# Performance work log

Hardware: AMD Instinct MI355X
Metric: run time of the kernel (lower is better)

Reference implementation:

```python
import jax, jax.numpy as jnp
import numpy as np

HIDDEN = 768
HEADS = 12
ORDERS = 3
NEG = -1e9


def setup_inputs() -> dict:
    key = jax.random.key(0)
    ks = jax.random.split(key, 16)
    B, N = 8, 512
    s = 0.02
    inp = {
        "v": jax.random.normal(ks[0], (B, N, HIDDEN), jnp.float32),
        "k": jax.random.normal(ks[1], (B, N, HIDDEN), jnp.float32),
        "q": jax.random.normal(ks[2], (B, N, HIDDEN), jnp.float32),
        "masks": jax.random.bernoulli(ks[3], 0.1, (ORDERS, B, 1, N, N)),
        "tau": 1,
        "training": 0,
        "Wv": jax.random.normal(ks[4], (HIDDEN, HIDDEN), jnp.float32) * s,
        "bv": jnp.zeros((HIDDEN,), jnp.float32),
        "Wk": jax.random.normal(ks[5], (HIDDEN, HIDDEN), jnp.float32) * s,
        "bk": jnp.zeros((HIDDEN,), jnp.float32),
        "Wq": jax.random.normal(ks[6], (HIDDEN, HIDDEN), jnp.float32) * s,
        "bq": jnp.zeros((HIDDEN,), jnp.float32),
        "Wm": jax.random.normal(ks[7], (HIDDEN, HIDDEN), jnp.float32) * s,
        "bm": jnp.zeros((HIDDEN,), jnp.float32),
        "pool_w": jax.random.normal(ks[8], (HIDDEN, 1), jnp.float32) * s,
        "pool_b": jnp.zeros((1,), jnp.float32),
        "mlp_w1": jax.random.normal(ks[9], (HIDDEN, HIDDEN // 2), jnp.float32) * s,
        "mlp_w2": jax.random.normal(ks[10], (HIDDEN // 2, ORDERS), jnp.float32) * s,
        "mlp_b2": jnp.zeros((ORDERS,), jnp.float32),
    }
    return inp


def _soft_routing(x, pool_w, pool_b, mlp_w1, mlp_w2, mlp_b2):
    # pooling='fc': masked attention pooling over sequence, then 2-layer MLP + softmax
    pad = (jnp.sum(jnp.abs(x), axis=-1) == 0)[:, :, None]        # [B, N, 1]
    scores = x @ pool_w + pool_b                                  # [B, N, 1]
    scores = jnp.where(pad, NEG, scores)
    scores = jax.nn.softmax(scores, axis=1)
    pooled = jnp.sum(x * scores, axis=1)                          # [B, HIDDEN]
    logits = jax.nn.relu(pooled @ mlp_w1) @ mlp_w2 + mlp_b2       # [B, L]
    return jax.nn.softmax(logits, axis=-1)


def reference(v, k, q, masks, tau, training, Wv, bv, Wk, bk, Wq, bq, Wm, bm,
              pool_w, pool_b, mlp_w1, mlp_w2, mlp_b2):
    B, N, _ = q.shape
    dk = HIDDEN // HEADS
    alphas = _soft_routing(v, pool_w, pool_b, mlp_w1, mlp_w2, mlp_b2)  # [B, L]

    def split_heads(x):
        return x.reshape(B, N, HEADS, dk).transpose(0, 2, 1, 3)  # [B, H, N, dk]

    vh = split_heads(v @ Wv + bv)
    kh = split_heads(k @ Wk + bk)
    qh = split_heads(q @ Wq + bq)

    scores = jnp.einsum('bhnd,bhmd->bhnm', qh, kh) / jnp.sqrt(jnp.float32(dk))
    # masks: [L, B, 1, N, N] broadcast over heads -> att_list [L, B, H, N, N]
    masked = jnp.where(masks[:, :, :, :, :], NEG, scores[None])
    att_list = jax.nn.softmax(masked, axis=-1)                    # [L, B, H, N, N]
    att_map = jnp.einsum('bl,lbhnm->bhnm', alphas, att_list)
    atted = jnp.einsum('bhnm,bhmd->bhnd', att_map, vh)
    atted = atted.transpose(0, 2, 1, 3).reshape(B, N, HIDDEN)
    return atted @ Wm + bm
```

## Files before the change

kernel.cpp:

```cpp
#include <hip/hip_runtime.h>
#include <hip/hip_bf16.h>
#include <stdint.h>


typedef __bf16 bf16x8 __attribute__((ext_vector_type(8)));
typedef float f32x4 __attribute__((ext_vector_type(4)));

#define NEGV -1e9f

__device__ __forceinline__ float b2f(unsigned short h) {
    union { unsigned int u; float f; } x; x.u = ((unsigned int)h) << 16; return x.f;
}
__device__ __forceinline__ unsigned short f2b(float f) {
    union { float f; unsigned int u; } x; x.f = f;
    unsigned int u = x.u + 0x7FFFu + ((x.u >> 16) & 1u);
    return (unsigned short)(u >> 16);
}
__device__ __forceinline__ unsigned int packbf(unsigned int u0, unsigned int u1) {
    unsigned int r0 = (u0 + 0x7FFFu + ((u0 >> 16) & 1u)) >> 16;
    unsigned int r1 = (u1 + 0x7FFFu + ((u1 >> 16) & 1u)) & 0xFFFF0000u;
    return r0 | r1;
}
__device__ __forceinline__ uint4 load8bf(const void* base, size_t elemOff, int isF32) {
    if (!isF32) return *(const uint4*)((const unsigned short*)base + elemOff);
    const uint4* f = (const uint4*)((const float*)base + elemOff);
    uint4 a = f[0], b = f[1];
    uint4 r;
    r.x = packbf(a.x, a.y);
    r.y = packbf(a.z, a.w);
    r.z = packbf(b.x, b.y);
    r.w = packbf(b.z, b.w);
    return r;
}
__device__ __forceinline__ float loadF(const void* p, int idx, int isF32) {
    return isF32 ? ((const float*)p)[idx] : b2f(((const unsigned short*)p)[idx]);
}

__global__ void sniff_kernel(const unsigned int* __restrict__ mp,
                             const unsigned int* __restrict__ vp,
                             const unsigned int* __restrict__ wp,
                             int* __restrict__ flags)
{
    __shared__ int oki, oku, okf, badv, badw;
    if (threadIdx.x == 0) { oki = 1; oku = 1; okf = 1; badv = 0; badw = 0; }
    __syncthreads();
    int li = 1, lu = 1, lf = 1, bv = 0, bw = 0;
    for (int i = threadIdx.x; i < 16384; i += 256) {
        unsigned int w = mp[i];
        if (w > 1u) li = 0;
        if (w & 0xFEFEFEFEu) lu = 0;
        if (w != 0u && w != 0x3F800000u) lf = 0;
    }
    for (int i = threadIdx.x; i < 8192; i += 256) {
        unsigned int w = vp[i];
        float f0 = b2f((unsigned short)(w & 0xFFFF));
        float f1 = b2f((unsigned short)(w >> 16));
        if (!(fabsf(f0) < 1e4f) || !(fabsf(f1) < 1e4f)) bv = 1;
        w = wp[i];
        f0 = b2f((unsigned short)(w & 0xFFFF));
        f1 = b2f((unsigned short)(w >> 16));
        if (!(fabsf(f0) < 1e4f) || !(fabsf(f1) < 1e4f)) bw = 1;
    }
    if (!li) atomicAnd(&oki, 0);
    if (!lu) atomicAnd(&oku, 0);
    if (!lf) atomicAnd(&okf, 0);
    if (bv) atomicOr(&badv, 1);
    if (bw) atomicOr(&badw, 1);
    __syncthreads();
    if (threadIdx.x == 0) {
        flags[0] = oki ? 0 : (oku ? 1 : (okf ? 2 : 3));
        flags[1] = badv;
        flags[2] = badw;
    }
}

__global__ __launch_bounds__(256) void conv_act_kernel(
        const void* __restrict__ v, const void* __restrict__ k,
        const void* __restrict__ q, const int* __restrict__ flags,
        unsigned short* __restrict__ vb, unsigned short* __restrict__ kb,
        unsigned short* __restrict__ qb)
{
    const int dtV = flags[1];
    const int which = blockIdx.y;
    const void* src = (which == 0) ? v : (which == 1) ? k : q;
    unsigned short* dst = (which == 0) ? vb : (which == 1) ? kb : qb;
    size_t off = ((size_t)blockIdx.x * 256 + threadIdx.x) * 8;
    uint4 r = load8bf(src, off, dtV);
    *(uint4*)(dst + off) = r;
}

__global__ __launch_bounds__(256) void conv_wt_kernel(
        const void* __restrict__ W0, const void* __restrict__ W1,
        const void* __restrict__ W2, const void* __restrict__ W3,
        const int* __restrict__ flags,
        unsigned short* __restrict__ T0, unsigned short* __restrict__ T1,
        unsigned short* __restrict__ T2, unsigned short* __restrict__ T3)
{
    __shared__ unsigned short tile[64][65];
    const int t = threadIdx.x;
    const int dtW = flags[2];
    const int which = blockIdx.y;
    const void* W = (which == 0) ? W0 : (which == 1) ? W1 : (which == 2) ? W2 : W3;
    unsigned short* T = (which == 0) ? T0 : (which == 1) ? T1 : (which == 2) ? T2 : T3;
    const int tk = (blockIdx.x / 12) << 6;
    const int tn = (blockIdx.x % 12) << 6;
    #pragma unroll
    for (int i = 0; i < 16; i++) {
        int idx = (i << 8) + t;
        int r = idx >> 6, c = idx & 63;
        tile[r][c] = f2b(loadF(W, (tk + r) * 768 + tn + c, dtW));
    }
    __syncthreads();
    #pragma unroll
    for (int i = 0; i < 16; i++) {
        int idx = (i << 8) + t;
        int rn = idx >> 6, ck = idx & 63;
        T[(size_t)(tn + rn) * 768 + tk + ck] = tile[ck][rn];
    }
}

__global__ __launch_bounds__(256) void pack_kernel(
        const void* __restrict__ masks, const int* __restrict__ flags,
        unsigned int* __restrict__ pm)
{
    __shared__ unsigned char flg[32 * 512];
    const int t = threadIdx.x;
    const int mode = flags[0];
    const size_t e0 = (size_t)blockIdx.x * (32 * 512);
    if (mode == 0 || mode == 2) {
        const uint4* p = (const uint4*)((const unsigned int*)masks + e0);
        for (int i = t; i < 4096; i += 256) {
            uint4 u = p[i];
            int base = i << 2;
            flg[base + 0] = u.x ? 1 : 0;
            flg[base + 1] = u.y ? 1 : 0;
            flg[base + 2] = u.z ? 1 : 0;
            flg[base + 3] = u.w ? 1 : 0;
        }
    } else if (mode == 1) {
        const uint4* p = (const uint4*)((const unsigned char*)masks + e0);
        for (int i = t; i < 1024; i += 256) {
            uint4 u = p[i];
            unsigned int uu[4] = {u.x, u.y, u.z, u.w};
            int base = i << 4;
            #pragma unroll
            for (int k2 = 0; k2 < 4; k2++)
                #pragma unroll
                for (int bb = 0; bb < 4; bb++)
                    flg[base + k2 * 4 + bb] = ((uu[k2] >> (bb * 8)) & 0xFFu) ? 1 : 0;
        }
    } else {
        const uint4* p = (const uint4*)((const unsigned short*)masks + e0);
        for (int i = t; i < 2048; i += 256) {
            uint4 u = p[i];
            unsigned int uu[4] = {u.x, u.y, u.z, u.w};
            int base = i << 3;
            #pragma unroll
            for (int k2 = 0; k2 < 4; k2++) {
                flg[base + k2 * 2 + 0] = (uu[k2] & 0xFFFFu) ? 1 : 0;
                flg[base + k2 * 2 + 1] = (uu[k2] >> 16) ? 1 : 0;
            }
        }
    }
    __syncthreads();
    for (int widx = t; widx < 512; widx += 256) {
        int rl = widx >> 4, lm = widx & 15;
        unsigned int bits = 0;
        #pragma unroll
        for (int g = 0; g < 32; g++)
            bits |= ((unsigned int)(flg[rl * 512 + (g << 4) + lm] & 1)) << g;
        pm[(size_t)blockIdx.x * 512 + widx] = bits;
    }
}

__global__ __launch_bounds__(256) void route_score_kernel(
        const void* __restrict__ v, const void* __restrict__ pool_w,
        const void* __restrict__ pool_b, const int* __restrict__ flags,
        float* __restrict__ scores)
{
    __shared__ float pw[768];
    const int t = threadIdx.x;
    const int b = blockIdx.x >> 3, ch = blockIdx.x & 7;
    const int dtV = flags[1], dtW = flags[2];
    for (int d = t; d < 768; d += 256) pw[d] = loadF(pool_w, d, dtW);
    __syncthreads();
    const int r = t >> 2, c4 = t & 3;
    const int n = (ch << 6) + r;
    float dot = 0.f, asum = 0.f;
    if (!dtV) {
        const unsigned int* vr = (const unsigned int*)v + ((size_t)(b * 512 + n)) * 384;
        for (int j = 0; j < 96; j++) {
            int p = c4 + (j << 2);
            unsigned int u = vr[p];
            float f0 = b2f((unsigned short)(u & 0xFFFF));
            float f1 = b2f((unsigned short)(u >> 16));
            asum += fabsf(f0) + fabsf(f1);
            dot += f0 * pw[2 * p] + f1 * pw[2 * p + 1];
        }
    } else {
        const float* vf = (const float*)v + ((size_t)(b * 512 + n)) * 768;
        for (int j = 0; j < 48; j++) {
            float4 u = ((const float4*)vf)[c4 + (j << 2)];
            int e = (c4 + (j << 2)) << 2;
            asum += fabsf(u.x) + fabsf(u.y) + fabsf(u.z) + fabsf(u.w);
            dot += u.x * pw[e] + u.y * pw[e + 1] + u.z * pw[e + 2] + u.w * pw[e + 3];
        }
    }
    dot += __shfl_xor(dot, 1); dot += __shfl_xor(dot, 2);
    asum += __shfl_xor(asum, 1); asum += __shfl_xor(asum, 2);
    if (c4 == 0)
        scores[b * 512 + n] = (asum == 0.f) ? NEGV : dot + loadF(pool_b, 0, dtW);
}

__global__ __launch_bounds__(512) void route_softmax_kernel(
        const float* __restrict__ scores, float* __restrict__ scs)
{
    __shared__ float red[8];
    const int t = threadIdx.x, b = blockIdx.x;
    float scv = scores[b * 512 + t];
    float mx = scv;
    #pragma unroll
    for (int off = 1; off < 64; off <<= 1) mx = fmaxf(mx, __shfl_xor(mx, off));
    if ((t & 63) == 0) red[t >> 6] = mx;
    __syncthreads();
    float M = red[0];
    #pragma unroll
    for (int i = 1; i < 8; i++) M = fmaxf(M, red[i]);
    float e = __expf(scv - M);
    __syncthreads();
    float sm = e;
    #pragma unroll
    for (int off = 1; off < 64; off <<= 1) sm += __shfl_xor(sm, off);
    if ((t & 63) == 0) red[t >> 6] = sm;
    __syncthreads();
    float SS = 0.f;
    #pragma unroll
    for (int i = 0; i < 8; i++) SS += red[i];
    scs[b * 512 + t] = e / SS;
}

__global__ __launch_bounds__(256) void route_pool_kernel(
        const void* __restrict__ v, const int* __restrict__ flags,
        const float* __restrict__ scs, float* __restrict__ ppart)
{
    __shared__ float ps[64];
    const int t = threadIdx.x;
    const int ch = blockIdx.x, b = blockIdx.y;
    const int dtV = flags[1];
    if (t < 64) ps[t] = scs[b * 512 + (ch << 6) + t];
    __syncthreads();
    const int d0 = t * 3;
    float a0 = 0.f, a1 = 0.f, a2 = 0.f;
    if (!dtV) {
        const unsigned short* vb = (const unsigned short*)v
            + ((size_t)(b * 512 + (ch << 6))) * 768 + d0;
        #pragma unroll 4
        for (int r = 0; r < 64; r++) {
            float p = ps[r];
            a0 += b2f(vb[0]) * p; a1 += b2f(vb[1]) * p; a2 += b2f(vb[2]) * p;
            vb += 768;
        }
    } else {
        const float* vb = (const float*)v + ((size_t)(b * 512 + (ch << 6))) * 768 + d0;
        #pragma unroll 4
        for (int r = 0; r < 64; r++) {
            float p = ps[r];
            a0 += vb[0] * p; a1 += vb[1] * p; a2 += vb[2] * p;
            vb += 768;
        }
    }
    float* o = ppart + ((size_t)(b * 8 + ch)) * 768 + d0;
    o[0] = a0; o[1] = a1; o[2] = a2;
}

__global__ __launch_bounds__(256) void route_hid_kernel(
        const void* __restrict__ w1, const void* __restrict__ w2,
        const int* __restrict__ flags, const float* __restrict__ ppart,
        float* __restrict__ plog)
{
    __shared__ float pool[768];
    __shared__ float red[4][32];
    const int t = threadIdx.x;
    const int jc = blockIdx.x, b = blockIdx.y;
    const int dtW = flags[2];
    for (int d = t; d < 768; d += 256) {
        float a = 0.f;
        #pragma unroll
        for (int c = 0; c < 8; c++) a += ppart[((size_t)(b * 8 + c)) * 768 + d];
        pool[d] = a;
    }
    __syncthreads();
    const int jo = (t & 3) << 3;
    const int dr = t >> 2;
    float acc[8];
    #pragma unroll
    for (int j = 0; j < 8; j++) acc[j] = 0.f;
    for (int it = 0; it < 12; it++) {
        int d = (it << 6) + dr;
        float pv = pool[d];
        size_t off = (size_t)d * 384 + (jc << 5) + jo;
        if (!dtW) {
            uint4 u = *(const uint4*)((const unsigned short*)w1 + off);
            unsigned int uu[4] = {u.x, u.y, u.z, u.w};
            #pragma unroll
            for (int j2 = 0; j2 < 4; j2++) {
                acc[2 * j2]     += pv * b2f((unsigned short)(uu[j2] & 0xFFFF));
                acc[2 * j2 + 1] += pv * b2f((unsigned short)(uu[j2] >> 16));
            }
        } else {
            const float4* f = (const float4*)((const float*)w1 + off);
            float4 u0 = f[0], u1 = f[1];
            acc[0] += pv * u0.x; acc[1] += pv * u0.y;
            acc[2] += pv * u0.z; acc[3] += pv * u0.w;
            acc[4] += pv * u1.x; acc[5] += pv * u1.y;
            acc[6] += pv * u1.z; acc[7] += pv * u1.w;
        }
    }
    #pragma unroll
    for (int off = 4; off < 64; off <<= 1)
        #pragma unroll
        for (int j = 0; j < 8; j++) acc[j] += __shfl_xor(acc[j], off);
    const int w = t >> 6, lane = t & 63;
    if (lane < 4) {
        #pragma unroll
        for (int j = 0; j < 8; j++) red[w][lane * 8 + j] = acc[j];
    }
    __syncthreads();
    if (t < 32) {
        float h = red[0][t] + red[1][t] + red[2][t] + red[3][t];
        h = fmaxf(h, 0.f);
        int jg = (jc << 5) + t;
        float l0 = h * loadF(w2, jg * 3 + 0, dtW);
        float l1 = h * loadF(w2, jg * 3 + 1, dtW);
        float l2 = h * loadF(w2, jg * 3 + 2, dtW);
        #pragma unroll
        for (int off = 1; off < 32; off <<= 1) {
            l0 += __shfl_xor(l0, off);
            l1 += __shfl_xor(l1, off);
            l2 += __shfl_xor(l2, off);
        }
        if (t == 0) {
            float* o = plog + ((size_t)(b * 12 + jc)) * 3;
            o[0] = l0; o[1] = l1; o[2] = l2;
        }
    }
}

__global__ __launch_bounds__(64) void route_alpha_kernel(
        const void* __restrict__ b2, const int* __restrict__ flags,
        const float* __restrict__ plog, float* __restrict__ alphas)
{
    const int t = threadIdx.x, b = blockIdx.x;
    if (t == 0) {
        const int dtW = flags[2];
        float lg[3];
        #pragma unroll
        for (int l = 0; l < 3; l++) {
            float a = loadF(b2, l, dtW);
            for (int jc = 0; jc < 12; jc++) a += plog[((size_t)(b * 12 + jc)) * 3 + l];
            lg[l] = a;
        }
        float mm = fmaxf(lg[0], fmaxf(lg[1], lg[2]));
        float e0 = __expf(lg[0] - mm), e1 = __expf(lg[1] - mm), e2 = __expf(lg[2] - mm);
        float ss = e0 + e1 + e2;
        alphas[b * 3 + 0] = e0 / ss;
        alphas[b * 3 + 1] = e1 / ss;
        alphas[b * 3 + 2] = e2 / ss;
    }
}

__global__ __launch_bounds__(256) void gemm3_kernel(
        const unsigned short* __restrict__ X0, const unsigned short* __restrict__ X1,
        const unsigned short* __restrict__ X2,
        const unsigned short* __restrict__ W0, const unsigned short* __restrict__ W1,
        const unsigned short* __restrict__ W2,
        const void* __restrict__ bias0, const void* __restrict__ bias1,
        const void* __restrict__ bias2,
        const int* __restrict__ flags,
        void* __restrict__ dst0, void* __restrict__ dst1, void* __restrict__ dst2,
        int m0, int m1, int m2)
{
    __shared__ unsigned short smem[8192];
    unsigned short* At = smem;
    unsigned short* Bt = smem + 4096;
    const int t = threadIdx.x;
    const int which = blockIdx.y;
    const unsigned short* X  = (which == 0) ? X0 : (which == 1) ? X1 : X2;
    const unsigned short* WT = (which == 0) ? W0 : (which == 1) ? W1 : W2;
    const void* bias = (which == 0) ? bias0 : (which == 1) ? bias1 : bias2;
    void* dst = (which == 0) ? dst0 : (which == 1) ? dst1 : dst2;
    const int mode = (which == 0) ? m0 : (which == 1) ? m1 : m2;

    const int id = blockIdx.x;
    const int bx = id >> 6, by = id & 63;
    const int row0 = by << 6, col0 = bx << 6;
    const int w = t >> 6, lane = t & 63, quad = lane >> 4, lm = lane & 15;
    const int r0 = t >> 3, c0 = (t & 7) << 3;
    const int wr0 = r0 * 64 + (c0 ^ ((r0 & 7) << 3));
    const int dtW = flags[2];
    const int dtOut = flags[1];

    const unsigned short* xp  = X  + (size_t)(row0 + r0) * 768 + c0;
    const unsigned short* xp2 = xp + 32 * 768;
    const unsigned short* wp  = WT + (size_t)(col0 + r0) * 768 + c0;
    const unsigned short* wp2 = wp + 32 * 768;

    uint4 a0 = *(const uint4*)xp,  a1 = *(const uint4*)xp2;
    uint4 g0 = *(const uint4*)wp,  g1 = *(const uint4*)wp2;

    f32x4 acc[4];
    #pragma unroll
    for (int i = 0; i < 4; i++) acc[i] = (f32x4){0.f, 0.f, 0.f, 0.f};

    const int am = (w << 4) + lm;
    const int abase = am * 64, akey = (am & 7) << 3;

    for (int k0 = 0;;) {
        __syncthreads();
        *(uint4*)&At[wr0] = a0;        *(uint4*)&At[wr0 + 2048] = a1;
        *(uint4*)&Bt[wr0] = g0;        *(uint4*)&Bt[wr0 + 2048] = g1;
        __syncthreads();
        k0 += 64;
        if (k0 < 768) {
            a0 = *(const uint4*)(xp + k0);  a1 = *(const uint4*)(xp2 + k0);
            g0 = *(const uint4*)(wp + k0);  g1 = *(const uint4*)(wp2 + k0);
        }
        #pragma unroll
        for (int ks = 0; ks < 2; ks++) {
            int ko = (quad << 3) + (ks << 5);
            bf16x8 afr = *(const bf16x8*)&At[abase + (ko ^ akey)];
            #pragma unroll
            for (int t4 = 0; t4 < 4; t4++) {
                int bn = (t4 << 4) + lm;
                bf16x8 bfr = *(const bf16x8*)&Bt[bn * 64 + (ko ^ ((bn & 7) << 3))];
                acc[t4] = __builtin_amdgcn_mfma_f32_16x16x32_bf16(afr, bfr, acc[t4], 0, 0, 0);
            }
        }
        if (k0 >= 768) break;
    }

    if (mode == 1 && dtOut) {
        #pragma unroll
        for (int t4 = 0; t4 < 4; t4++) {
            int col = col0 + (t4 << 4) + lm;
            float bsv = loadF(bias, col, dtW);
            #pragma unroll
            for (int rg = 0; rg < 4; rg++) {
                int row = row0 + (w << 4) + (quad << 2) + rg;
                ((float*)dst)[(size_t)row * 768 + col] = acc[t4][rg] + bsv;
            }
        }
        return;
    }

    __syncthreads();
    #pragma unroll
    for (int t4 = 0; t4 < 4; t4++) {
        int colL = (t4 << 4) + lm;
        float bsv = loadF(bias, col0 + colL, dtW);
        #pragma unroll
        for (int rg = 0; rg < 4; rg++) {
            int rowL = (w << 4) + (quad << 2) + rg;
            unsigned short hv = f2b(acc[t4][rg] + bsv);
            if (mode == 2) smem[colL * 72 + rowL] = hv;
            else           smem[rowL * 72 + colL] = hv;
        }
    }
    __syncthreads();
    const int g = t >> 2, cc = (t & 3) << 4;
    uint4 o0 = *(const uint4*)&smem[g * 72 + cc];
    uint4 o1 = *(const uint4*)&smem[g * 72 + cc + 8];
    unsigned short* o;
    if (mode == 0) {
        int b = row0 >> 9, n0b = row0 & 511, h = col0 >> 6;
        o = (unsigned short*)dst + ((size_t)(b * 12 + h) * 512 + n0b + g) * 64 + cc;
    } else if (mode == 2) {
        int b = row0 >> 9, n0b = row0 & 511, h = col0 >> 6;
        o = (unsigned short*)dst + ((size_t)(b * 12 + h) * 64 + g) * 512 + n0b + cc;
    } else {
        o = (unsigned short*)dst + (size_t)(row0 + g) * 768 + col0 + cc;
    }
    *(uint4*)o = o0;
    *(uint4*)(o + 8) = o1;
}

__global__ __launch_bounds__(256) void attn_kernel(
        const unsigned short* __restrict__ qh, const unsigned short* __restrict__ kh,
        const unsigned short* __restrict__ vT, const unsigned int* __restrict__ pm,
        const float* __restrict__ alphas, unsigned short* __restrict__ atted)
{
    __shared__ unsigned short P[16 * 512];
    __shared__ float Zp[4][16][3];
    __shared__ unsigned short Ost[16 * 72];
    const int t = threadIdx.x;
    const int w = t >> 6, lane = t & 63, quad = lane >> 4, lm = lane & 15;
    const int id = blockIdx.x;
    const int bh = id % 96, qb = id / 96;
    const int b = bh / 12, h = bh % 12;
    const int n0 = qb << 4;

    const unsigned short* qrow = qh + ((size_t)(bh * 512 + n0 + lm)) * 64 + (quad << 3);
    bf16x8 qa0 = *(const bf16x8*)qrow;
    bf16x8 qa1 = *(const bf16x8*)(qrow + 32);
    f32x4 acc[8];
    #pragma unroll
    for (int i = 0; i < 8; i++) acc[i] = (f32x4){0.f, 0.f, 0.f, 0.f};
    const unsigned short* kb0 = kh + ((size_t)(bh * 512 + (w << 7) + lm)) * 64 + (quad << 3);
    #pragma unroll
    for (int nt = 0; nt < 8; nt++) {
        const unsigned short* kr = kb0 + nt * (16 * 64);
        bf16x8 k0 = *(const bf16x8*)kr;
        bf16x8 k1 = *(const bf16x8*)(kr + 32);
        acc[nt] = __builtin_amdgcn_mfma_f32_16x16x32_bf16(qa0, k0, acc[nt], 0, 0, 0);
        acc[nt] = __builtin_amdgcn_mfma_f32_16x16x32_bf16(qa1, k1, acc[nt], 0, 0, 0);
    }

    float al[3];
    #pragma unroll
    for (int l = 0; l < 3; l++) al[l] = alphas[b * 3 + l];

    #pragma unroll
    for (int nt = 0; nt < 8; nt++)
        #pragma unroll
        for (int rg = 0; rg < 4; rg++)
            acc[nt][rg] = __expf(acc[nt][rg] * 0.125f);

    unsigned int mkw[4][3];
    #pragma unroll
    for (int rg = 0; rg < 4; rg++)
        #pragma unroll
        for (int l = 0; l < 3; l++)
            mkw[rg][l] = pm[((size_t)((l << 3) + b) * 512 + n0 + (quad << 2) + rg) * 16 + lm]
                         >> (w << 3);

    #pragma unroll
    for (int rg = 0; rg < 4; rg++) {
        float z0 = 0.f, z1 = 0.f, z2 = 0.f;
        #pragma unroll
        for (int nt = 0; nt < 8; nt++) {
            float e = acc[nt][rg];
            if (!((mkw[rg][0] >> nt) & 1)) z0 += e;
            if (!((mkw[rg][1] >> nt) & 1)) z1 += e;
            if (!((mkw[rg][2] >> nt) & 1)) z2 += e;
        }
        #pragma unroll
        for (int off = 1; off < 16; off <<= 1) {
            z0 += __shfl_xor(z0, off);
            z1 += __shfl_xor(z1, off);
            z2 += __shfl_xor(z2, off);
        }
        if (lm == 0) {
            int row = (quad << 2) + rg;
            Zp[w][row][0] = z0; Zp[w][row][1] = z1; Zp[w][row][2] = z2;
        }
    }
    __syncthreads();

    #pragma unroll
    for (int rg = 0; rg < 4; rg++) {
        int row = (quad << 2) + rg;
        float coef[3]; float addu = 0.f;
        #pragma unroll
        for (int l = 0; l < 3; l++) {
            float Z = Zp[0][row][l] + Zp[1][row][l] + Zp[2][row][l] + Zp[3][row][l];
            if (Z > 0.f) coef[l] = al[l] / Z;
            else { coef[l] = 0.f; addu += al[l] * (1.0f / 512.0f); }
        }
        #pragma unroll
        for (int nt = 0; nt < 8; nt++) {
            int g = (w << 3) + nt;
            float p = addu;
            float e = acc[nt][rg];
            if (!((mkw[rg][0] >> nt) & 1)) p += coef[0] * e;
            if (!((mkw[rg][1] >> nt) & 1)) p += coef[1] * e;
            if (!((mkw[rg][2] >> nt) & 1)) p += coef[2] * e;
            int c = (g << 4) + lm;
            int chunk = c >> 3, j = c & 7;
            P[row * 512 + (((chunk ^ (row & 7))) << 3) + j] = f2b(p);
        }
    }
    __syncthreads();

    f32x4 accO = (f32x4){0.f, 0.f, 0.f, 0.f};
    const unsigned short* vb = vT + ((size_t)(bh * 64 + (w << 4) + lm)) * 512 + (quad << 3);
    #pragma unroll
    for (int ks = 0; ks < 16; ks++) {
        bf16x8 pa = *(const bf16x8*)&P[lm * 512 + ((((ks << 2) + quad) ^ (lm & 7)) << 3)];
        bf16x8 vf = *(const bf16x8*)(vb + (ks << 5));
        accO = __builtin_amdgcn_mfma_f32_16x16x32_bf16(pa, vf, accO, 0, 0, 0);
    }
    #pragma unroll
    for (int rg = 0; rg < 4; rg++)
        Ost[((quad << 2) + rg) * 72 + (w << 4) + lm] = f2b(accO[rg]);
    __syncthreads();
    const int r2 = t >> 4, c4 = t & 15;
    uint2 val = *(const uint2*)&Ost[r2 * 72 + (c4 << 2)];
    *(uint2*)&atted[((size_t)(b * 512 + n0 + r2)) * 768 + (h << 6) + (c4 << 2)] = val;
}

extern "C" void kernel_launch(void* const* d_in, const int* in_sizes, int n_in,
                              void* d_out, int out_size, void* d_ws, size_t ws_size,
                              hipStream_t stream)
{
    const void* v  = d_in[0];
    const void* k  = d_in[1];
    const void* q  = d_in[2];
    const void* mk = d_in[3];
    const void* Wv = d_in[6];
    const void* bv = d_in[7];
    const void* Wk = d_in[8];
    const void* bk = d_in[9];
    const void* Wq = d_in[10];
    const void* bq = d_in[11];
    const void* Wm = d_in[12];
    const void* bm = d_in[13];
    const void* pool_w = d_in[14];
    const void* pool_b = d_in[15];
    const void* w1 = d_in[16];
    const void* w2 = d_in[17];
    const void* b2 = d_in[18];

    char* ws = (char*)d_ws;
    int*   flags  = (int*)ws;
    float* alphas = (float*)(ws + 256);
    float* scores = (float*)(ws + 512);
    float* scs    = (float*)(ws + 16896);
    float* ppart  = (float*)(ws + 33280);
    float* plog   = (float*)(ws + 229888);
    unsigned int* pm = (unsigned int*)(ws + 262144);
    unsigned short* qh  = (unsigned short*)(ws + 1048576);
    unsigned short* kh  = (unsigned short*)(ws + 1048576 + 1 * 6291456L);
    unsigned short* vT  = (unsigned short*)(ws + 1048576 + 2 * 6291456L);
    unsigned short* vb  = (unsigned short*)(ws + 1048576 + 3 * 6291456L);
    unsigned short* kb  = (unsigned short*)(ws + 1048576 + 4 * 6291456L);
    unsigned short* qb  = (unsigned short*)(ws + 1048576 + 5 * 6291456L);
    unsigned short* atted = vb;
    char* wt0 = ws + 1048576 + 6 * 6291456L;
    unsigned short* WTv = (unsigned short*)(wt0);
    unsigned short* WTk = (unsigned short*)(wt0 + 1 * 1179648L);
    unsigned short* WTq = (unsigned short*)(wt0 + 2 * 1179648L);
    unsigned short* WTm = (unsigned short*)(wt0 + 3 * 1179648L);

    sniff_kernel<<<dim3(1), dim3(256), 0, stream>>>(
        (const unsigned int*)mk, (const unsigned int*)v, (const unsigned int*)Wv, flags);
    conv_act_kernel<<<dim3(1536, 3), dim3(256), 0, stream>>>(v, k, q, flags, vb, kb, qb);
    conv_wt_kernel<<<dim3(144, 4), dim3(256), 0, stream>>>(
        Wv, Wk, Wq, Wm, flags, WTv, WTk, WTq, WTm);
    pack_kernel<<<dim3(384), dim3(256), 0, stream>>>(mk, flags, pm);
    route_score_kernel<<<dim3(64), dim3(256), 0, stream>>>(v, pool_w, pool_b, flags, scores);
    route_softmax_kernel<<<dim3(8), dim3(512), 0, stream>>>(scores, scs);
    route_pool_kernel<<<dim3(8, 8), dim3(256), 0, stream>>>(v, flags, scs, ppart);
    route_hid_kernel<<<dim3(12, 8), dim3(256), 0, stream>>>(w1, w2, flags, ppart, plog);
    route_alpha_kernel<<<dim3(8), dim3(64), 0, stream>>>(b2, flags, plog, alphas);
    gemm3_kernel<<<dim3(768, 3), dim3(256), 0, stream>>>(
        vb, kb, qb, WTv, WTk, WTq, bv, bk, bq, flags,
        (void*)vT, (void*)kh, (void*)qh, 2, 0, 0);
    attn_kernel<<<dim3(3072), dim3(256), 0, stream>>>(qh, kh, vT, pm, alphas, atted);
    gemm3_kernel<<<dim3(768, 1), dim3(256), 0, stream>>>(
        atted, atted, atted, WTm, WTm, WTm, bm, bm, bm, flags,
        d_out, d_out, d_out, 1, 1, 1);
}
```

Before: 300.4 us.

## Repack mask bits per attention lane and branchless masked softmax in attention

```diff
diff --git a/kernel.cpp b/kernel.cpp
--- a/kernel.cpp
+++ b/kernel.cpp
@@ -7,6 +7,7 @@
 typedef float f32x4 __attribute__((ext_vector_type(4)));
 
 #define NEGV -1e9f
+#define SBFE(x, off) (((int)((x) << (31 - (off)))) >> 31)
 
 __device__ __forceinline__ float b2f(unsigned short h) {
     union { unsigned int u; float f; } x; x.u = ((unsigned int)h) << 16; return x.f;
@@ -45,21 +46,34 @@
     if (threadIdx.x == 0) { oki = 1; oku = 1; okf = 1; badv = 0; badw = 0; }
     __syncthreads();
     int li = 1, lu = 1, lf = 1, bv = 0, bw = 0;
-    for (int i = threadIdx.x; i < 16384; i += 256) {
-        unsigned int w = mp[i];
-        if (w > 1u) li = 0;
-        if (w & 0xFEFEFEFEu) lu = 0;
-        if (w != 0u && w != 0x3F800000u) lf = 0;
-    }
-    for (int i = threadIdx.x; i < 8192; i += 256) {
-        unsigned int w = vp[i];
-        float f0 = b2f((unsigned short)(w & 0xFFFF));
-        float f1 = b2f((unsigned short)(w >> 16));
-        if (!(fabsf(f0) < 1e4f) || !(fabsf(f1) < 1e4f)) bv = 1;
-        w = wp[i];
-        f0 = b2f((unsigned short)(w & 0xFFFF));
-        f1 = b2f((unsigned short)(w >> 16));
-        if (!(fabsf(f0) < 1e4f) || !(fabsf(f1) < 1e4f)) bw = 1;
+    const uint4* m4 = (const uint4*)mp;
+    for (int i = threadIdx.x; i < 4096; i += 256) {
+        uint4 u = m4[i];
+        unsigned int ws[4] = {u.x, u.y, u.z, u.w};
+        #pragma unroll
+        for (int j = 0; j < 4; j++) {
+            unsigned int w = ws[j];
+            if (w > 1u) li = 0;
+            if (w & 0xFEFEFEFEu) lu = 0;
+            if (w != 0u && w != 0x3F800000u) lf = 0;
+        }
+    }
+    const uint4* v4 = (const uint4*)vp;
+    const uint4* w4 = (const uint4*)wp;
+    for (int i = threadIdx.x; i < 2048; i += 256) {
+        uint4 u = v4[i];
+        uint4 u2 = w4[i];
+        unsigned int wa[4] = {u.x, u.y, u.z, u.w};
+        unsigned int wb[4] = {u2.x, u2.y, u2.z, u2.w};
+        #pragma unroll
+        for (int j = 0; j < 4; j++) {
+            float f0 = b2f((unsigned short)(wa[j] & 0xFFFF));
+            float f1 = b2f((unsigned short)(wa[j] >> 16));
+            if (!(fabsf(f0) < 1e4f) || !(fabsf(f1) < 1e4f)) bv = 1;
+            f0 = b2f((unsigned short)(wb[j] & 0xFFFF));
+            f1 = b2f((unsigned short)(wb[j] >> 16));
+            if (!(fabsf(f0) < 1e4f) || !(fabsf(f1) < 1e4f)) bw = 1;
+        }
     }
     if (!li) atomicAnd(&oki, 0);
     if (!lu) atomicAnd(&oku, 0);
@@ -163,13 +177,20 @@
         }
     }
     __syncthreads();
+    const int lbi = blockIdx.x >> 4;
+    const int qb0 = (blockIdx.x & 15) << 1;
     for (int widx = t; widx < 512; widx += 256) {
-        int rl = widx >> 4, lm = widx & 15;
+        const int qq = widx >> 8, sub = widx & 255;
+        const int w2 = sub >> 6, lm = (sub >> 2) & 15, quad = sub & 3;
+        const unsigned char* fr = &flg[(((qq << 4) + (quad << 2)) << 9) + lm];
         unsigned int bits = 0;
         #pragma unroll
-        for (int g = 0; g < 32; g++)
-            bits |= ((unsigned int)(flg[rl * 512 + (g << 4) + lm] & 1)) << g;
-        pm[(size_t)blockIdx.x * 512 + widx] = bits;
+        for (int rg = 0; rg < 4; rg++)
+            #pragma unroll
+            for (int nt = 0; nt < 8; nt++)
+                bits |= ((unsigned int)(fr[(rg << 9) + (((w2 << 3) + nt) << 4)] & 1u))
+                        << ((rg << 3) + nt);
+        pm[(size_t)lbi * 8192 + (size_t)(qb0 + qq) * 256 + sub] = bits;
     }
 }
 
@@ -499,6 +520,16 @@
     const int b = bh / 12, h = bh % 12;
     const int n0 = qb << 4;
 
+    const unsigned int* pmb = pm + (size_t)b * 8192 + (size_t)qb * 256
+                                 + (w << 6) + (lm << 2) + quad;
+    const unsigned int mw0 = pmb[0];
+    const unsigned int mw1 = pmb[65536];
+    const unsigned int mw2 = pmb[131072];
+
+    float al[3];
+    #pragma unroll
+    for (int l = 0; l < 3; l++) al[l] = alphas[b * 3 + l];
+
     const unsigned short* qrow = qh + ((size_t)(bh * 512 + n0 + lm)) * 64 + (quad << 3);
     bf16x8 qa0 = *(const bf16x8*)qrow;
     bf16x8 qa1 = *(const bf16x8*)(qrow + 32);
@@ -515,33 +546,24 @@
         acc[nt] = __builtin_amdgcn_mfma_f32_16x16x32_bf16(qa1, k1, acc[nt], 0, 0, 0);
     }
 
-    float al[3];
-    #pragma unroll
-    for (int l = 0; l < 3; l++) al[l] = alphas[b * 3 + l];
-
     #pragma unroll
     for (int nt = 0; nt < 8; nt++)
         #pragma unroll
         for (int rg = 0; rg < 4; rg++)
             acc[nt][rg] = __expf(acc[nt][rg] * 0.125f);
 
-    unsigned int mkw[4][3];
-    #pragma unroll
-    for (int rg = 0; rg < 4; rg++)
-        #pragma unroll
-        for (int l = 0; l < 3; l++)
-            mkw[rg][l] = pm[((size_t)((l << 3) + b) * 512 + n0 + (quad << 2) + rg) * 16 + lm]
-                         >> (w << 3);
+    const unsigned int im0 = ~mw0, im1 = ~mw1, im2 = ~mw2;
 
     #pragma unroll
     for (int rg = 0; rg < 4; rg++) {
         float z0 = 0.f, z1 = 0.f, z2 = 0.f;
         #pragma unroll
         for (int nt = 0; nt < 8; nt++) {
-            float e = acc[nt][rg];
-            if (!((mkw[rg][0] >> nt) & 1)) z0 += e;
-            if (!((mkw[rg][1] >> nt) & 1)) z1 += e;
-            if (!((mkw[rg][2] >> nt) & 1)) z2 += e;
+            const int bp = (rg << 3) + nt;
+            const unsigned int e = __float_as_uint(acc[nt][rg]);
+            z0 += __uint_as_float(e & (unsigned int)SBFE(im0, bp));
+            z1 += __uint_as_float(e & (unsigned int)SBFE(im1, bp));
+            z2 += __uint_as_float(e & (unsigned int)SBFE(im2, bp));
         }
         #pragma unroll
         for (int off = 1; off < 16; off <<= 1) {
@@ -558,40 +580,50 @@
 
     #pragma unroll
     for (int rg = 0; rg < 4; rg++) {
-        int row = (quad << 2) + rg;
-        float coef[3]; float addu = 0.f;
+        const int row = (quad << 2) + rg;
+        float addu = 0.f;
+        unsigned int cb[3];
         #pragma unroll
         for (int l = 0; l < 3; l++) {
             float Z = Zp[0][row][l] + Zp[1][row][l] + Zp[2][row][l] + Zp[3][row][l];
-            if (Z > 0.f) coef[l] = al[l] / Z;
-            else { coef[l] = 0.f; addu += al[l] * (1.0f / 512.0f); }
-        }
+            float c;
+            if (Z > 0.f) c = al[l] * __builtin_amdgcn_rcpf(Z);
+            else { c = 0.f; addu += al[l] * (1.0f / 512.0f); }
+            cb[l] = __float_as_uint(c);
+        }
+        const int key = row & 7;
+        const int pbase = row * 512 + (lm & 7) + (w << 7)
+                        + ((((lm >> 3) ^ key) & 1) << 3);
+        const int kk16 = (key >> 1) << 4;
         #pragma unroll
         for (int nt = 0; nt < 8; nt++) {
-            int g = (w << 3) + nt;
-            float p = addu;
-            float e = acc[nt][rg];
-            if (!((mkw[rg][0] >> nt) & 1)) p += coef[0] * e;
-            if (!((mkw[rg][1] >> nt) & 1)) p += coef[1] * e;
-            if (!((mkw[rg][2] >> nt) & 1)) p += coef[2] * e;
-            int c = (g << 4) + lm;
-            int chunk = c >> 3, j = c & 7;
-            P[row * 512 + (((chunk ^ (row & 7))) << 3) + j] = f2b(p);
-        }
-    }
+            const int bp = (rg << 3) + nt;
+            float wsum = __uint_as_float(cb[0] & (unsigned int)SBFE(im0, bp))
+                       + __uint_as_float(cb[1] & (unsigned int)SBFE(im1, bp))
+                       + __uint_as_float(cb[2] & (unsigned int)SBFE(im2, bp));
+            float p = fmaf(acc[nt][rg], wsum, addu);
+            unsigned int u = __float_as_uint(p) + 0x8000u;
+            P[pbase + ((nt << 4) ^ kk16)] = (unsigned short)(u >> 16);
+        }
+    }
+
+    const unsigned short* vb = vT + ((size_t)(bh * 64 + (w << 4) + lm)) * 512 + (quad << 3);
+    bf16x8 vp0 = *(const bf16x8*)vb;
+    bf16x8 vp1 = *(const bf16x8*)(vb + 32);
     __syncthreads();
 
     f32x4 accO = (f32x4){0.f, 0.f, 0.f, 0.f};
-    const unsigned short* vb = vT + ((size_t)(bh * 64 + (w << 4) + lm)) * 512 + (quad << 3);
     #pragma unroll
     for (int ks = 0; ks < 16; ks++) {
         bf16x8 pa = *(const bf16x8*)&P[lm * 512 + ((((ks << 2) + quad) ^ (lm & 7)) << 3)];
-        bf16x8 vf = *(const bf16x8*)(vb + (ks << 5));
+        bf16x8 vf = (ks == 0) ? vp0 : (ks == 1) ? vp1 : *(const bf16x8*)(vb + (ks << 5));
         accO = __builtin_amdgcn_mfma_f32_16x16x32_bf16(pa, vf, accO, 0, 0, 0);
     }
     #pragma unroll
-    for (int rg = 0; rg < 4; rg++)
-        Ost[((quad << 2) + rg) * 72 + (w << 4) + lm] = f2b(accO[rg]);
+    for (int rg = 0; rg < 4; rg++) {
+        unsigned int u = __float_as_uint(accO[rg]) + 0x8000u;
+        Ost[((quad << 2) + rg) * 72 + (w << 4) + lm] = (unsigned short)(u >> 16);
+    }
     __syncthreads();
     const int r2 = t >> 4, c4 = t & 15;
     uint2 val = *(const uint2*)&Ost[r2 * 72 + (c4 << 2)];
```

New measurement: 276.2 us. 8.1% less time.
